# Performance work log

Measured on AMD Instinct MI355X. Metric: run time of the kernel, lower is better.

## Reference

```python
import jax, jax.numpy as jnp
import numpy as np

IN_DIM, HID, T, B = 512, 1024, 64, 2048


def setup_inputs() -> dict:
    key = jax.random.key(0)
    ks = jax.random.split(key, 9)
    s_in = 1.0 / np.sqrt(IN_DIM)
    s_h = 1.0 / np.sqrt(HID)
    return {
        "inputs": jax.random.normal(ks[0], (T, B, IN_DIM), jnp.float32),
        "W1": jax.random.normal(ks[1], (HID, IN_DIM), jnp.float32) * s_in,
        "b1": jax.random.normal(ks[2], (HID,), jnp.float32) * s_in,
        "W_ih": jax.random.normal(ks[3], (3 * HID, HID), jnp.float32) * s_h,
        "b_ih": jax.random.normal(ks[4], (3 * HID,), jnp.float32) * s_h,
        "W_hh": jax.random.normal(ks[5], (3 * HID, HID), jnp.float32) * s_h,
        "b_hh": jax.random.normal(ks[6], (3 * HID,), jnp.float32) * s_h,
        "W3": jax.random.normal(ks[7], (1, HID), jnp.float32) * s_h,
        "b3": jax.random.normal(ks[8], (1,), jnp.float32) * s_h,
        "max_t": T,
        "bs": B,
    }


def reference(inputs, W1, b1, W_ih, b_ih, W_hh, b_hh, W3, b3, max_t, bs):
    x = inputs.reshape(max_t, bs, -1)                      # (T, B, in)
    # fc1 + relu for all timesteps at once (no h dependency)
    x = jax.nn.relu(jnp.einsum('tbi,hi->tbh', x, W1) + b1)  # (T, B, H)
    # precompute input-side GRU gates for all steps
    gx_all = jnp.einsum('tbh,gh->tbg', x, W_ih) + b_ih      # (T, B, 3H)

    def step(h, gx):
        gh = h @ W_hh.T + b_hh                              # (B, 3H)
        xr, xz, xn = jnp.split(gx, 3, axis=-1)
        hr, hz, hn = jnp.split(gh, 3, axis=-1)
        r = jax.nn.sigmoid(xr + hr)
        z = jax.nn.sigmoid(xz + hz)
        n = jnp.tanh(xn + r * hn)
        h_new = (1.0 - z) * n + z * h                       # PyTorch GRUCell update
        return h_new, h_new

    h0 = jnp.zeros((bs, W_hh.shape[1]), inputs.dtype)
    _, hs = jax.lax.scan(step, h0, gx_all)                  # hs: (T, B, H)
    q = jnp.einsum('tbh,oh->tbo', hs, W3) + b3              # (T, B, 1)
    # faithful to torch: raw reshape (NOT transpose) of (T,B,1) -> (B,T,1)
    return q.reshape(bs, max_t, 1)
```

## Files before the change

kernel.cpp:

```cpp
#include <hip/hip_runtime.h>

#define TT   64
#define BB   2048
#define IND  512
#define HH   1024
#define G3   3072
#define TBM  (TT*BB)

typedef short  short8 __attribute__((ext_vector_type(8)));
typedef float  f32x4  __attribute__((ext_vector_type(4)));

__device__ __forceinline__ unsigned short f2bf(float x) {
  unsigned int u = __float_as_uint(x);
  u += 0x7FFFu + ((u >> 16) & 1u);
  return (unsigned short)(u >> 16);
}
__device__ __forceinline__ float bf2f(unsigned short u) {
  return __uint_as_float(((unsigned int)u) << 16);
}

__device__ __forceinline__ void async16(const void* g, void* l) {
  __builtin_amdgcn_global_load_lds(
      (__attribute__((address_space(1))) void*)(void*)g,
      (__attribute__((address_space(3))) void*)l, 16, 0, 0);
}

__global__ void cast_bf16_kernel(const float* __restrict__ src,
                                 unsigned short* __restrict__ dst, int n) {
  int stride = gridDim.x * blockDim.x;
  for (int i = blockIdx.x * blockDim.x + threadIdx.x; i * 8 < n; i += stride) {
    int o = i * 8;
    float4 a = *(const float4*)(src + o);
    float4 b = *(const float4*)(src + o + 4);
    ushort4 lo; lo.x = f2bf(a.x); lo.y = f2bf(a.y); lo.z = f2bf(a.z); lo.w = f2bf(a.w);
    ushort4 hi; hi.x = f2bf(b.x); hi.y = f2bf(b.y); hi.z = f2bf(b.z); hi.w = f2bf(b.w);
    *(ushort4*)(dst + o)     = lo;
    *(ushort4*)(dst + o + 4) = hi;
  }
}

__global__ void init_out_kernel(float* __restrict__ out, const float* __restrict__ b3, int n) {
  float v = b3[0];
  for (int i = blockIdx.x * blockDim.x + threadIdx.x; i < n; i += gridDim.x * blockDim.x)
    out[i] = v;
}

template <int RELU>
__global__ __launch_bounds__(256, 2) void gemm_bf16(
    const unsigned short* __restrict__ A,
    const unsigned short* __restrict__ Bw,
    const float* __restrict__ bias,
    unsigned short* __restrict__ C,
    int M, int N, int K) {
  __shared__ __align__(16) unsigned short As[128 * 32];
  __shared__ __align__(16) unsigned short Bs[128 * 32];
  const int tid = threadIdx.x;
  const int w = tid >> 6, l = tid & 63;
  const int wr = w >> 1, wc = w & 1;
  const int lq = l >> 4, lr = l & 15;
  const long m0 = (long)blockIdx.y * 128;
  const int  n0 = blockIdx.x * 128;
  const int srow = l >> 2, scol = (l & 3) * 8;

  f32x4 acc[4][4] = {};

  const unsigned short* ga = A  + (m0 + w * 32 + srow) * K + scol;
  const unsigned short* gb = Bw + (long)(n0 + w * 32 + srow) * K + scol;
  unsigned short* lA = &As[(w * 32) * 32];
  unsigned short* lB = &Bs[(w * 32) * 32];

  for (int k0 = 0; k0 < K; k0 += 32) {
    async16(ga,          lA);
    async16(ga + 16 * K, lA + 16 * 32);
    async16(gb,          lB);
    async16(gb + 16 * K, lB + 16 * 32);
    ga += 32; gb += 32;
    __syncthreads();
    short8 af[4], bfv[4];
#pragma unroll
    for (int mf = 0; mf < 4; mf++)
      af[mf] = *(const short8*)&As[(wr * 64 + mf * 16 + lr) * 32 + 8 * lq];
#pragma unroll
    for (int nf = 0; nf < 4; nf++)
      bfv[nf] = *(const short8*)&Bs[(wc * 64 + nf * 16 + lr) * 32 + 8 * lq];
#pragma unroll
    for (int mf = 0; mf < 4; mf++)
#pragma unroll
      for (int nf = 0; nf < 4; nf++)
        acc[mf][nf] = __builtin_amdgcn_mfma_f32_16x16x32_bf16(af[mf], bfv[nf], acc[mf][nf], 0, 0, 0);
    __syncthreads();
  }

#pragma unroll
  for (int nf = 0; nf < 4; nf++) {
    int col = n0 + wc * 64 + nf * 16 + lr;
    float bv = bias[col];
#pragma unroll
    for (int mf = 0; mf < 4; mf++) {
      long row = m0 + wr * 64 + mf * 16 + 4 * lq;
#pragma unroll
      for (int r = 0; r < 4; r++) {
        float v = acc[mf][nf][r] + bv;
        if (RELU) v = fmaxf(v, 0.f);
        C[(row + r) * N + col] = f2bf(v);
      }
    }
  }
}

__global__ __launch_bounds__(256, 2) void gru_step(
    const unsigned short* __restrict__ hprev_bf,
    const float* __restrict__ hprev_f,
    float* __restrict__ hnext_f,
    unsigned short* __restrict__ hnext_bf,
    const unsigned short* __restrict__ Whh,
    const unsigned short* __restrict__ gx,
    const float* __restrict__ bhh,
    const float* __restrict__ W3,
    float* __restrict__ out,
    int lt, int t) {
  __shared__ __align__(16) unsigned short As[64 * 32];
  __shared__ __align__(16) unsigned short Bs[3][64 * 32];
  const int tid = threadIdx.x;
  const int w = tid >> 6, l = tid & 63;
  const int wr = w >> 1, wc = w & 1;
  const int lq = l >> 4, lr = l & 15;
  const int m0 = blockIdx.y * 64;
  const int n0 = blockIdx.x * 64;
  const int srow = l >> 2, scol = (l & 3) * 8;

  f32x4 acc[3][2][2] = {};

  const unsigned short* ga = hprev_bf + (m0 + w * 16 + srow) * HH + scol;
  unsigned short* lA = &As[(w * 16) * 32];

  for (int k0 = 0; k0 < HH; k0 += 32) {
    async16(ga, lA);
#pragma unroll
    for (int g = 0; g < 3; g++) {
      const unsigned short* gb =
          Whh + (long)(g * HH + n0 + w * 16 + srow) * HH + k0 + scol;
      async16(gb, &Bs[g][(w * 16) * 32]);
    }
    ga += 32;
    __syncthreads();
    short8 af[2];
#pragma unroll
    for (int mf = 0; mf < 2; mf++)
      af[mf] = *(const short8*)&As[(wr * 32 + mf * 16 + lr) * 32 + 8 * lq];
#pragma unroll
    for (int g = 0; g < 3; g++)
#pragma unroll
      for (int nf = 0; nf < 2; nf++) {
        short8 bfr = *(const short8*)&Bs[g][(wc * 32 + nf * 16 + lr) * 32 + 8 * lq];
#pragma unroll
        for (int mf = 0; mf < 2; mf++)
          acc[g][mf][nf] = __builtin_amdgcn_mfma_f32_16x16x32_bf16(af[mf], bfr, acc[g][mf][nf], 0, 0, 0);
      }
    __syncthreads();
  }

  float qp[2][4] = {};
#pragma unroll
  for (int nf = 0; nf < 2; nf++) {
    int n = n0 + wc * 32 + nf * 16 + lr;
    float bhr = bhh[n], bhz = bhh[HH + n], bhn = bhh[2 * HH + n];
    float w3v = W3[n];
#pragma unroll
    for (int mf = 0; mf < 2; mf++) {
      int mrow = m0 + wr * 32 + mf * 16 + 4 * lq;
#pragma unroll
      for (int r = 0; r < 4; r++) {
        int m = mrow + r;
        long gxb = ((long)lt * BB + m) * G3 + n;
        float xr = bf2f(gx[gxb]);
        float xz = bf2f(gx[gxb + HH]);
        float xn = bf2f(gx[gxb + 2 * HH]);
        float ghr = acc[0][mf][nf][r] + bhr;
        float ghz = acc[1][mf][nf][r] + bhz;
        float ghn = acc[2][mf][nf][r] + bhn;
        float rg = 1.f / (1.f + __expf(-(xr + ghr)));
        float zg = 1.f / (1.f + __expf(-(xz + ghz)));
        float ng = tanhf(xn + rg * ghn);
        float hp = hprev_f[(long)m * HH + n];
        float hv = (1.f - zg) * ng + zg * hp;
        hnext_f[(long)m * HH + n] = hv;
        hnext_bf[(long)m * HH + n] = f2bf(hv);
        qp[mf][r] += hv * w3v;
      }
    }
  }
#pragma unroll
  for (int mf = 0; mf < 2; mf++)
#pragma unroll
    for (int r = 0; r < 4; r++) {
      float v = qp[mf][r];
      v += __shfl_xor(v, 1);
      v += __shfl_xor(v, 2);
      v += __shfl_xor(v, 4);
      v += __shfl_xor(v, 8);
      if (lr == 0) {
        int m = m0 + wr * 32 + mf * 16 + 4 * lq + r;
        atomicAdd(&out[t * BB + m], v);
      }
    }
}

extern "C" void kernel_launch(void* const* d_in, const int* in_sizes, int n_in,
                              void* d_out, int out_size, void* d_ws, size_t ws_size,
                              hipStream_t stream) {
  const float* inputs = (const float*)d_in[0];
  const float* W1     = (const float*)d_in[1];
  const float* b1     = (const float*)d_in[2];
  const float* W_ih   = (const float*)d_in[3];
  const float* b_ih   = (const float*)d_in[4];
  const float* W_hh   = (const float*)d_in[5];
  const float* b_hh   = (const float*)d_in[6];
  const float* W3     = (const float*)d_in[7];
  const float* b3     = (const float*)d_in[8];
  float* out = (float*)d_out;

  const long FIXED = 38797312L;
  const long PER   = 18874368L;
  int TC = 64;
  while (TC > 1 && FIXED + (long)TC * PER > (long)ws_size) TC >>= 1;

  char* ws = (char*)d_ws;
  unsigned short* whhb = (unsigned short*)ws;
  unsigned short* wihb = whhb + 3145728;
  unsigned short* w1b  = wihb + 3145728;
  float* hf0 = (float*)(ws + 13631488L);
  float* hf1 = hf0 + (long)BB * HH;
  unsigned short* hb0 = (unsigned short*)(ws + 30408704L);
  unsigned short* hb1 = hb0 + (long)BB * HH;
  unsigned short* gxc   = (unsigned short*)(ws + FIXED);
  unsigned short* xc    = gxc + (long)TC * BB * G3;
  unsigned short* inbfc = xc  + (long)TC * BB * HH;

  cast_bf16_kernel<<<512, 256, 0, stream>>>(W1,   w1b,  HH * IND);
  cast_bf16_kernel<<<1024, 256, 0, stream>>>(W_ih, wihb, G3 * HH);
  cast_bf16_kernel<<<1024, 256, 0, stream>>>(W_hh, whhb, G3 * HH);
  hipMemsetAsync(hf0, 0, (long)BB * HH * 4, stream);
  hipMemsetAsync(hb0, 0, (long)BB * HH * 2, stream);
  init_out_kernel<<<512, 256, 0, stream>>>(out, b3, TBM);

  for (int c = 0; c < TT; c += TC) {
    const int rows = TC * BB;
    cast_bf16_kernel<<<2048, 256, 0, stream>>>(
        inputs + (long)c * BB * IND, inbfc, rows * IND);
    gemm_bf16<1><<<dim3(HH / 128, rows / 128), 256, 0, stream>>>(
        inbfc, w1b, b1, xc, rows, HH, IND);
    gemm_bf16<0><<<dim3(G3 / 128, rows / 128), 256, 0, stream>>>(
        xc, wihb, b_ih, gxc, rows, G3, HH);
    for (int lt = 0; lt < TC; lt++) {
      const int t = c + lt;
      const unsigned short* hbr = (t & 1) ? hb1 : hb0;
      const float*          hfr = (t & 1) ? hf1 : hf0;
      float*                hfw = (t & 1) ? hf0 : hf1;
      unsigned short*       hbw = (t & 1) ? hb0 : hb1;
      gru_step<<<dim3(HH / 64, BB / 64), 256, 0, stream>>>(
          hbr, hfr, hfw, hbw, whhb, gxc, b_hh, W3, out, lt, t);
    }
  }
}
```

Measured before the change: 3.843 ms.

## Persistent cooperative GRU kernel with grid sync and double-buffered swizzled GEMM tiles

Replaces the per-timestep gru_step launches with one cooperative persistent kernel per chunk that loops over timesteps and uses grid.sync between steps. It also enlarges the GRU tile to 128x64 with 512 threads, a 64-wide K step and double-buffered, XOR-swizzled LDS staging. The projection GEMM gets the same double buffering and swizzle plus a grouped block-index remap for L2 locality. The aim is to remove launch overhead, overlap loads with MFMA and cut LDS bank conflicts. In exchange, each step now pays a grid-wide barrier, and the larger LDS footprint may lower occupancy.

```diff
diff --git a/kernel.cpp b/kernel.cpp
--- a/kernel.cpp
+++ b/kernel.cpp
@@ -1,4 +1,7 @@
 #include <hip/hip_runtime.h>
+#include <hip/hip_cooperative_groups.h>
+
+namespace cg = cooperative_groups;
 
 #define TT   64
 #define BB   2048
@@ -52,43 +55,69 @@
     const float* __restrict__ bias,
     unsigned short* __restrict__ C,
     int M, int N, int K) {
-  __shared__ __align__(16) unsigned short As[128 * 32];
-  __shared__ __align__(16) unsigned short Bs[128 * 32];
+  __shared__ __align__(16) unsigned short As[2][128 * 64];
+  __shared__ __align__(16) unsigned short Bs[2][128 * 64];
   const int tid = threadIdx.x;
   const int w = tid >> 6, l = tid & 63;
   const int wr = w >> 1, wc = w & 1;
   const int lq = l >> 4, lr = l & 15;
-  const long m0 = (long)blockIdx.y * 128;
-  const int  n0 = blockIdx.x * 128;
-  const int srow = l >> 2, scol = (l & 3) * 8;
+  const int gX = gridDim.x;
+  int fid = blockIdx.y * gX + blockIdx.x;
+  int cpx = (gX * gridDim.y) >> 3;
+  int fid2 = (fid & 7) * cpx + (fid >> 3);
+  const int  n0 = (fid2 % gX) * 128;
+  const long m0 = (long)(fid2 / gX) * 128;
+  const int cswz = ((l & 7) ^ (l >> 3)) * 8;
+  int co[2];
+#pragma unroll
+  for (int kk = 0; kk < 2; kk++)
+    co[kk] = (((kk * 64 + lq * 16) ^ ((lr & 7) << 4)) >> 1);
 
   f32x4 acc[4][4] = {};
-
-  const unsigned short* ga = A  + (m0 + w * 32 + srow) * K + scol;
-  const unsigned short* gb = Bw + (long)(n0 + w * 32 + srow) * K + scol;
-  unsigned short* lA = &As[(w * 32) * 32];
-  unsigned short* lB = &Bs[(w * 32) * 32];
-
-  for (int k0 = 0; k0 < K; k0 += 32) {
-    async16(ga,          lA);
-    async16(ga + 16 * K, lA + 16 * 32);
-    async16(gb,          lB);
-    async16(gb + 16 * K, lB + 16 * 32);
-    ga += 32; gb += 32;
+  const int NK = K >> 6;
+
+  auto STAGE = [&](int buf, int kb) {
+    const int k0 = kb << 6;
+#pragma unroll
+    for (int j = 0; j < 8; j++) {
+      if (w < 2) {
+        const int r0 = (w * 8 + j) * 8;
+        async16(A + (m0 + r0 + (l >> 3)) * K + k0 + cswz, &As[buf][r0 * 64]);
+      } else {
+        const int r0 = ((w - 2) * 8 + j) * 8;
+        async16(Bw + (long)(n0 + r0 + (l >> 3)) * K + k0 + cswz, &Bs[buf][r0 * 64]);
+      }
+    }
+  };
+
+  STAGE(0, 0);
+  for (int kb = 0; kb < NK; kb++) {
     __syncthreads();
-    short8 af[4], bfv[4];
-#pragma unroll
-    for (int mf = 0; mf < 4; mf++)
-      af[mf] = *(const short8*)&As[(wr * 64 + mf * 16 + lr) * 32 + 8 * lq];
-#pragma unroll
-    for (int nf = 0; nf < 4; nf++)
-      bfv[nf] = *(const short8*)&Bs[(wc * 64 + nf * 16 + lr) * 32 + 8 * lq];
-#pragma unroll
-    for (int mf = 0; mf < 4; mf++)
-#pragma unroll
-      for (int nf = 0; nf < 4; nf++)
-        acc[mf][nf] = __builtin_amdgcn_mfma_f32_16x16x32_bf16(af[mf], bfv[nf], acc[mf][nf], 0, 0, 0);
-    __syncthreads();
+    if (kb + 1 < NK) STAGE((kb + 1) & 1, kb + 1);
+    const unsigned short* Ac = As[kb & 1];
+    const unsigned short* Bc = Bs[kb & 1];
+    short8 af[4][2], bfv[4][2];
+#pragma unroll
+    for (int mf = 0; mf < 4; mf++) {
+      const int row = wr * 64 + mf * 16 + lr;
+#pragma unroll
+      for (int kk = 0; kk < 2; kk++)
+        af[mf][kk] = *(const short8*)&Ac[row * 64 + co[kk]];
+    }
+#pragma unroll
+    for (int nf = 0; nf < 4; nf++) {
+      const int row = wc * 64 + nf * 16 + lr;
+#pragma unroll
+      for (int kk = 0; kk < 2; kk++)
+        bfv[nf][kk] = *(const short8*)&Bc[row * 64 + co[kk]];
+    }
+#pragma unroll
+    for (int kk = 0; kk < 2; kk++)
+#pragma unroll
+      for (int mf = 0; mf < 4; mf++)
+#pragma unroll
+        for (int nf = 0; nf < 4; nf++)
+          acc[mf][nf] = __builtin_amdgcn_mfma_f32_16x16x32_bf16(af[mf][kk], bfv[nf][kk], acc[mf][nf], 0, 0, 0);
   }
 
 #pragma unroll
@@ -108,102 +137,137 @@
   }
 }
 
-__global__ __launch_bounds__(256, 2) void gru_step(
-    const unsigned short* __restrict__ hprev_bf,
-    const float* __restrict__ hprev_f,
-    float* __restrict__ hnext_f,
-    unsigned short* __restrict__ hnext_bf,
+__global__ __launch_bounds__(512, 2) void gru_persist(
     const unsigned short* __restrict__ Whh,
     const unsigned short* __restrict__ gx,
     const float* __restrict__ bhh,
     const float* __restrict__ W3,
     float* __restrict__ out,
-    int lt, int t) {
-  __shared__ __align__(16) unsigned short As[64 * 32];
-  __shared__ __align__(16) unsigned short Bs[3][64 * 32];
+    float* __restrict__ hfA, float* __restrict__ hfB,
+    unsigned short* __restrict__ hbA, unsigned short* __restrict__ hbB,
+    int c, int TC) {
+  __shared__ __align__(16) unsigned short As[2][128 * 64];
+  __shared__ __align__(16) unsigned short Bs[2][3][64 * 64];
+  cg::grid_group grid = cg::this_grid();
   const int tid = threadIdx.x;
   const int w = tid >> 6, l = tid & 63;
   const int wr = w >> 1, wc = w & 1;
   const int lq = l >> 4, lr = l & 15;
-  const int m0 = blockIdx.y * 64;
-  const int n0 = blockIdx.x * 64;
-  const int srow = l >> 2, scol = (l & 3) * 8;
-
-  f32x4 acc[3][2][2] = {};
-
-  const unsigned short* ga = hprev_bf + (m0 + w * 16 + srow) * HH + scol;
-  unsigned short* lA = &As[(w * 16) * 32];
-
-  for (int k0 = 0; k0 < HH; k0 += 32) {
-    async16(ga, lA);
-#pragma unroll
-    for (int g = 0; g < 3; g++) {
-      const unsigned short* gb =
-          Whh + (long)(g * HH + n0 + w * 16 + srow) * HH + k0 + scol;
-      async16(gb, &Bs[g][(w * 16) * 32]);
-    }
-    ga += 32;
-    __syncthreads();
-    short8 af[2];
+  const int bid = blockIdx.x;
+  const int n0 = (bid & 15) * 64;
+  const int m0 = (bid >> 4) * 128;
+  const int cswz = ((l & 7) ^ (l >> 3)) * 8;
+  int co[2];
+#pragma unroll
+  for (int kk = 0; kk < 2; kk++)
+    co[kk] = (((kk * 64 + lq * 16) ^ ((lr & 7) << 4)) >> 1);
+
+  for (int lt = 0; lt < TC; lt++) {
+    const int t = c + lt;
+    const unsigned short* hpb = (t & 1) ? hbB : hbA;
+    const float*          hpf = (t & 1) ? hfB : hfA;
+    float*                hnf = (t & 1) ? hfA : hfB;
+    unsigned short*       hnb = (t & 1) ? hbA : hbB;
+
+    f32x4 acc[3][2][2] = {};
+
+    auto STAGE = [&](int buf, int kb) {
+      const int k0 = kb << 6;
+#pragma unroll
+      for (int j = 0; j < 5; j++) {
+        const int ci = w * 5 + j;
+        if (ci < 16) {
+          const int r0 = ci * 8;
+          async16(hpb + (long)(m0 + r0 + (l >> 3)) * HH + k0 + cswz, &As[buf][r0 * 64]);
+        } else {
+          const int g = (ci - 16) >> 3, r0 = ((ci - 16) & 7) * 8;
+          async16(Whh + (long)(g * HH + n0 + r0 + (l >> 3)) * HH + k0 + cswz,
+                  &Bs[buf][g][r0 * 64]);
+        }
+      }
+    };
+
+    STAGE(0, 0);
+    for (int kb = 0; kb < 16; kb++) {
+      __syncthreads();
+      if (kb < 15) STAGE((kb + 1) & 1, kb + 1);
+      const unsigned short* Ac = As[kb & 1];
+      short8 af[2][2];
+#pragma unroll
+      for (int mf = 0; mf < 2; mf++) {
+        const int row = wr * 32 + mf * 16 + lr;
+#pragma unroll
+        for (int kk = 0; kk < 2; kk++)
+          af[mf][kk] = *(const short8*)&Ac[row * 64 + co[kk]];
+      }
+#pragma unroll
+      for (int g = 0; g < 3; g++) {
+        const unsigned short* Bc = Bs[kb & 1][g];
+        short8 bfv[2][2];
+#pragma unroll
+        for (int nf = 0; nf < 2; nf++) {
+          const int row = wc * 32 + nf * 16 + lr;
+#pragma unroll
+          for (int kk = 0; kk < 2; kk++)
+            bfv[nf][kk] = *(const short8*)&Bc[row * 64 + co[kk]];
+        }
+#pragma unroll
+        for (int kk = 0; kk < 2; kk++)
+#pragma unroll
+          for (int mf = 0; mf < 2; mf++)
+#pragma unroll
+            for (int nf = 0; nf < 2; nf++)
+              acc[g][mf][nf] = __builtin_amdgcn_mfma_f32_16x16x32_bf16(af[mf][kk], bfv[nf][kk], acc[g][mf][nf], 0, 0, 0);
+      }
+    }
+
+    float qp[2][4] = {};
+#pragma unroll
+    for (int nf = 0; nf < 2; nf++) {
+      const int n = n0 + wc * 32 + nf * 16 + lr;
+      const float bhr = bhh[n], bhz = bhh[HH + n], bhn = bhh[2 * HH + n];
+      const float w3v = W3[n];
+#pragma unroll
+      for (int mf = 0; mf < 2; mf++) {
+        const int mrow = m0 + wr * 32 + mf * 16 + 4 * lq;
+#pragma unroll
+        for (int r = 0; r < 4; r++) {
+          const int m = mrow + r;
+          const long gxb = ((long)lt * BB + m) * G3 + n;
+          float xr = bf2f(gx[gxb]);
+          float xz = bf2f(gx[gxb + HH]);
+          float xn = bf2f(gx[gxb + 2 * HH]);
+          float ghr = acc[0][mf][nf][r] + bhr;
+          float ghz = acc[1][mf][nf][r] + bhz;
+          float ghn = acc[2][mf][nf][r] + bhn;
+          float rg = 1.f / (1.f + __expf(-(xr + ghr)));
+          float zg = 1.f / (1.f + __expf(-(xz + ghz)));
+          float ng = tanhf(xn + rg * ghn);
+          float hp = hpf[(long)m * HH + n];
+          float hv = (1.f - zg) * ng + zg * hp;
+          hnf[(long)m * HH + n] = hv;
+          hnb[(long)m * HH + n] = f2bf(hv);
+          qp[mf][r] += hv * w3v;
+        }
+      }
+    }
 #pragma unroll
     for (int mf = 0; mf < 2; mf++)
-      af[mf] = *(const short8*)&As[(wr * 32 + mf * 16 + lr) * 32 + 8 * lq];
-#pragma unroll
-    for (int g = 0; g < 3; g++)
-#pragma unroll
-      for (int nf = 0; nf < 2; nf++) {
-        short8 bfr = *(const short8*)&Bs[g][(wc * 32 + nf * 16 + lr) * 32 + 8 * lq];
-#pragma unroll
-        for (int mf = 0; mf < 2; mf++)
-          acc[g][mf][nf] = __builtin_amdgcn_mfma_f32_16x16x32_bf16(af[mf], bfr, acc[g][mf][nf], 0, 0, 0);
-      }
-    __syncthreads();
-  }
-
-  float qp[2][4] = {};
-#pragma unroll
-  for (int nf = 0; nf < 2; nf++) {
-    int n = n0 + wc * 32 + nf * 16 + lr;
-    float bhr = bhh[n], bhz = bhh[HH + n], bhn = bhh[2 * HH + n];
-    float w3v = W3[n];
-#pragma unroll
-    for (int mf = 0; mf < 2; mf++) {
-      int mrow = m0 + wr * 32 + mf * 16 + 4 * lq;
 #pragma unroll
       for (int r = 0; r < 4; r++) {
-        int m = mrow + r;
-        long gxb = ((long)lt * BB + m) * G3 + n;
-        float xr = bf2f(gx[gxb]);
-        float xz = bf2f(gx[gxb + HH]);
-        float xn = bf2f(gx[gxb + 2 * HH]);
-        float ghr = acc[0][mf][nf][r] + bhr;
-        float ghz = acc[1][mf][nf][r] + bhz;
-        float ghn = acc[2][mf][nf][r] + bhn;
-        float rg = 1.f / (1.f + __expf(-(xr + ghr)));
-        float zg = 1.f / (1.f + __expf(-(xz + ghz)));
-        float ng = tanhf(xn + rg * ghn);
-        float hp = hprev_f[(long)m * HH + n];
-        float hv = (1.f - zg) * ng + zg * hp;
-        hnext_f[(long)m * HH + n] = hv;
-        hnext_bf[(long)m * HH + n] = f2bf(hv);
-        qp[mf][r] += hv * w3v;
-      }
-    }
-  }
-#pragma unroll
-  for (int mf = 0; mf < 2; mf++)
-#pragma unroll
-    for (int r = 0; r < 4; r++) {
-      float v = qp[mf][r];
-      v += __shfl_xor(v, 1);
-      v += __shfl_xor(v, 2);
-      v += __shfl_xor(v, 4);
-      v += __shfl_xor(v, 8);
-      if (lr == 0) {
-        int m = m0 + wr * 32 + mf * 16 + 4 * lq + r;
-        atomicAdd(&out[t * BB + m], v);
-      }
-    }
+        float v = qp[mf][r];
+        v += __shfl_xor(v, 1);
+        v += __shfl_xor(v, 2);
+        v += __shfl_xor(v, 4);
+        v += __shfl_xor(v, 8);
+        if (lr == 0) {
+          int m = m0 + wr * 32 + mf * 16 + 4 * lq + r;
+          atomicAdd(&out[t * BB + m], v);
+        }
+      }
+    __threadfence();
+    grid.sync();
+  }
 }
 
 extern "C" void kernel_launch(void* const* d_in, const int* in_sizes, int n_in,
@@ -252,14 +316,18 @@
         inbfc, w1b, b1, xc, rows, HH, IND);
     gemm_bf16<0><<<dim3(G3 / 128, rows / 128), 256, 0, stream>>>(
         xc, wihb, b_ih, gxc, rows, G3, HH);
-    for (int lt = 0; lt < TC; lt++) {
-      const int t = c + lt;
-      const unsigned short* hbr = (t & 1) ? hb1 : hb0;
-      const float*          hfr = (t & 1) ? hf1 : hf0;
-      float*                hfw = (t & 1) ? hf0 : hf1;
-      unsigned short*       hbw = (t & 1) ? hb0 : hb1;
-      gru_step<<<dim3(HH / 64, BB / 64), 256, 0, stream>>>(
-          hbr, hfr, hfw, hbw, whhb, gxc, b_hh, W3, out, lt, t);
-    }
-  }
-}
+
+    const unsigned short* a_whh = whhb;
+    const unsigned short* a_gx  = gxc;
+    const float* a_bhh = b_hh;
+    const float* a_w3  = W3;
+    float* a_out = out;
+    float* a_hfA = hf0; float* a_hfB = hf1;
+    unsigned short* a_hbA = hb0; unsigned short* a_hbB = hb1;
+    int a_c = c, a_tc = TC;
+    void* args[] = {&a_whh, &a_gx, &a_bhh, &a_w3, &a_out,
+                    &a_hfA, &a_hfB, &a_hbA, &a_hbB, &a_c, &a_tc};
+    hipLaunchCooperativeKernel(reinterpret_cast<void*>(gru_persist),
+                               dim3(256), dim3(512), args, 0, stream);
+  }
+}
```

Result: slower. 8.220 ms (+113.9%).
